# Performance work log

Hardware: AMD Instinct MI355X
Metric: run time of the kernel (lower is better)

Reference implementation:

```python
import jax, jax.numpy as jnp
import numpy as np

N_ROLES = 6
EPS = 1e-5

def _ln(x, scale, bias):
    m = jnp.mean(x, axis=-1, keepdims=True)
    v = jnp.var(x, axis=-1, keepdims=True)
    return (x - m) * jax.lax.rsqrt(v + EPS) * scale + bias

def setup_inputs() -> dict:
    key = jax.random.key(0)
    ks = jax.random.split(key, 20)
    T, B, D_OBS, H, A = 32, 1024, 256, 512, 32
    inp = {
        'rnn_states': jax.random.normal(ks[0], (B, H), jnp.float32),
        'obs': jax.random.normal(ks[1], (T, B, D_OBS), jnp.float32),
        'resets': jnp.zeros((T, B), jnp.float32),
        'available_actions': jnp.ones((T, B, A), jnp.float32),
        'role_ids': jax.random.randint(ks[2], (T, B), 0, N_ROLES, jnp.int32),
        # feature norm over obs_dim
        'fn_scale': jnp.ones((D_OBS,), jnp.float32),
        'fn_bias': jnp.zeros((D_OBS,), jnp.float32),
        # base MLP: obs_dim->512->512, each followed by LayerNorm
        'W0': jax.random.normal(ks[3], (D_OBS, H), jnp.float32) * 0.02,
        'b0': jnp.zeros((H,), jnp.float32),
        'ln0_scale': jnp.ones((H,), jnp.float32),
        'ln0_bias': jnp.zeros((H,), jnp.float32),
        'W1': jax.random.normal(ks[4], (H, H), jnp.float32) * 0.02,
        'b1': jnp.zeros((H,), jnp.float32),
        'ln1_scale': jnp.ones((H,), jnp.float32),
        'ln1_bias': jnp.zeros((H,), jnp.float32),
        # per-role routes: obs_dim->128->H (stacked over roles)
        'Wr0': jax.random.normal(ks[5], (N_ROLES, D_OBS, 128), jnp.float32) * 0.02,
        'br0': jnp.zeros((N_ROLES, 128), jnp.float32),
        'Wr1': jax.random.normal(ks[6], (N_ROLES, 128, H), jnp.float32) * 0.02,
        'br1': jnp.zeros((N_ROLES, H), jnp.float32),
        # per-role heads: H->64->32->action_dim (stacked over roles)
        'Wh0': jax.random.normal(ks[7], (N_ROLES, H, 64), jnp.float32) * 0.02,
        'bh0': jnp.zeros((N_ROLES, 64), jnp.float32),
        'Wh1': jax.random.normal(ks[8], (N_ROLES, 64, 32), jnp.float32) * 0.02,
        'bh1': jnp.zeros((N_ROLES, 32), jnp.float32),
        'Wh2': jax.random.normal(ks[9], (N_ROLES, 32, A), jnp.float32) * 0.02,
        'bh2': jnp.zeros((N_ROLES, A), jnp.float32),
    }
    return inp

def _gather_by_role(all_values, role_ids):
    # all_values: (K, T, B, F); role_ids: (T, B) -> (T, B, F)
    idx = role_ids[None, :, :, None].astype(jnp.int32)
    return jnp.take_along_axis(all_values, idx, axis=0)[0]

def reference(rnn_states, obs, resets, available_actions, role_ids,
              fn_scale, fn_bias, W0, b0, ln0_scale, ln0_bias,
              W1, b1, ln1_scale, ln1_bias,
              Wr0, br0, Wr1, br1,
              Wh0, bh0, Wh1, bh1, Wh2, bh2):
    # feature normalization on raw obs
    obs_n = _ln(obs, fn_scale, fn_bias)
    # shared base MLP (relu + LayerNorm after each Dense)
    e = _ln(jax.nn.relu(obs_n @ W0 + b0), ln0_scale, ln0_bias)
    e = _ln(jax.nn.relu(e @ W1 + b1), ln1_scale, ln1_bias)
    # per-role pre-GRU residual routes on (normalized) obs
    r = jax.nn.relu(jnp.einsum('tbi,kih->ktbh', obs_n, Wr0) + br0[:, None, None, :])
    r = jax.nn.relu(jnp.einsum('ktbh,kho->ktbo', r, Wr1) + br1[:, None, None, :])
    e = e + _gather_by_role(r, role_ids)
    # no recurrent policy configured: rnn_states pass through
    # per-role heads -> all logits (K, T, B, A)
    h = jax.nn.relu(jnp.einsum('tbh,khf->ktbf', e, Wh0) + bh0[:, None, None, :])
    h = jax.nn.relu(jnp.einsum('ktbf,kfg->ktbg', h, Wh1) + bh1[:, None, None, :])
    all_logits = jnp.einsum('ktbg,kga->ktba', h, Wh2) + bh2[:, None, None, :]
    logits = _gather_by_role(all_logits, role_ids)
    logits = jnp.where(available_actions > 0.5, logits, jnp.full_like(logits, -1e10))
    return rnn_states, logits
```

## Files before the change

### kernel.cpp

```cpp
#include <hip/hip_runtime.h>
#include <stdint.h>

typedef unsigned short u16;
typedef unsigned int u32;

using bf16x8 = __attribute__((ext_vector_type(8))) short;
using f32x4  = __attribute__((ext_vector_type(4))) float;

#define DEVINL __device__ __forceinline__

DEVINL float b2f(u16 u) { return __builtin_bit_cast(float, (u32)u << 16); }
DEVINL u16 f2b(float f) {
  u32 u = __builtin_bit_cast(u32, f);
  u += 0x7FFFu + ((u >> 16) & 1u);
  return (u16)(u >> 16);
}

DEVINL void gll16(const u16* src, u16* dst) {
  __builtin_amdgcn_global_load_lds(
      (const __attribute__((address_space(1))) void*)(uintptr_t)src,
      (__attribute__((address_space(3))) void*)(uintptr_t)dst, 16, 0, 0);
}

DEVINL void tp_tile(const float* __restrict__ s, u16* __restrict__ d,
                    int R, int C, int bx, int by, int z)
{
  __shared__ u16 tile[32][33];
  const size_t mstride = (size_t)R * C;
  s += (size_t)z * mstride;
  d += (size_t)z * mstride;
  int r0 = bx * 32, c0 = by * 32;
  int tx = threadIdx.x & 31, ty = threadIdx.x >> 5;
#pragma unroll
  for (int i = 0; i < 32; i += 8)
    tile[ty + i][tx] = f2b(s[(size_t)(r0 + ty + i) * C + (c0 + tx)]);
  __syncthreads();
#pragma unroll
  for (int i = 0; i < 32; i += 8)
    d[(size_t)(c0 + ty + i) * R + (r0 + tx)] = tile[tx][ty + i];
}

__global__ __launch_bounds__(256) void transpose_all(
    const float* W0, const float* W1, const float* Wr0, const float* Wr1, const float* Wh0,
    u16* W0t, u16* W1t, u16* Wr0t, u16* Wr1t, u16* Wh0t)
{
  int b = blockIdx.x;
  if (b < 128)      {            tp_tile(W0, W0t, 256, 512, b % 8,  b / 8, 0); }
  else if (b < 384) { b -= 128;  tp_tile(W1, W1t, 512, 512, b % 16, b / 16, 0); }
  else if (b < 576) { b -= 384;  int t = b / 8;  tp_tile(Wr0, Wr0t, 256, 128, b % 8,  t % 4,  t / 4); }
  else if (b < 960) { b -= 576;  int t = b / 4;  tp_tile(Wr1, Wr1t, 128, 512, b % 4,  t % 16, t / 16); }
  else              { b -= 960;  int t = b / 16; tp_tile(Wh0, Wh0t, 512, 64,  b % 16, t % 2,  t / 2); }
}

__global__ __launch_bounds__(256) void ln_f32_256(
    const float* __restrict__ X, const float* __restrict__ sc,
    const float* __restrict__ bi, u16* __restrict__ Y, int nrows)
{
  constexpr int D = 256, PER = 4;
  int lane = threadIdx.x & 63;
  int row = blockIdx.x * 4 + (threadIdx.x >> 6);
  if (row >= nrows) return;
  const float* xr = X + (size_t)row * D + lane * PER;
  float x[PER] __attribute__((aligned(16)));
  *(float4*)x = *(const float4*)xr;
  float s = 0.f, s2 = 0.f;
#pragma unroll
  for (int p = 0; p < PER; ++p) { s += x[p]; s2 += x[p] * x[p]; }
#pragma unroll
  for (int o = 32; o > 0; o >>= 1) { s += __shfl_xor(s, o, 64); s2 += __shfl_xor(s2, o, 64); }
  float m = s * (1.f / D);
  float v = s2 * (1.f / D) - m * m;
  float inv = rsqrtf(v + 1e-5f);
  u16 yu[PER] __attribute__((aligned(8)));
#pragma unroll
  for (int p = 0; p < PER; ++p)
    yu[p] = f2b((x[p] - m) * inv * sc[lane * PER + p] + bi[lane * PER + p]);
  *(uint2*)(Y + (size_t)row * D + lane * PER) = *(uint2*)yu;
}

#define NROLE 6
__global__ __launch_bounds__(256) void role_count(
    const int* __restrict__ rid, int* __restrict__ blkCnt)
{
  __shared__ int h[NROLE];
  if (threadIdx.x < NROLE) h[threadIdx.x] = 0;
  __syncthreads();
  int i = blockIdx.x * 256 + threadIdx.x;
  atomicAdd(&h[rid[i]], 1);
  __syncthreads();
  if (threadIdx.x < NROLE) blkCnt[blockIdx.x * NROLE + threadIdx.x] = h[threadIdx.x];
}

__global__ __launch_bounds__(256) void role_scan(
    const int* __restrict__ blkCnt, int* __restrict__ blkBase,
    int* __restrict__ baseArr, int* __restrict__ cntArr)
{
  __shared__ int c[128 * NROLE];
  __shared__ int bb[128 * NROLE];
  __shared__ int sbase[NROLE], scnt[NROLE];
  for (int i = threadIdx.x; i < 128 * NROLE; i += 256) c[i] = blkCnt[i];
  __syncthreads();
  if (threadIdx.x < NROLE) {
    int k = threadIdx.x, run = 0;
    for (int b = 0; b < 128; ++b) { bb[b * NROLE + k] = run; run += c[b * NROLE + k]; }
    scnt[k] = run;
  }
  __syncthreads();
  if (threadIdx.x == 0) {
    int r = 0;
    for (int k = 0; k < NROLE; ++k) { sbase[k] = r; r += scnt[k]; }
  }
  __syncthreads();
  if (threadIdx.x < NROLE) { baseArr[threadIdx.x] = sbase[threadIdx.x]; cntArr[threadIdx.x] = scnt[threadIdx.x]; }
  for (int i = threadIdx.x; i < 128 * NROLE; i += 256)
    blkBase[i] = bb[i] + sbase[i % NROLE];
}

__global__ __launch_bounds__(256) void role_fill(
    const int* __restrict__ rid, const int* __restrict__ blkBase, int* __restrict__ bucket)
{
  __shared__ int h[NROLE];
  if (threadIdx.x < NROLE) h[threadIdx.x] = 0;
  __syncthreads();
  int i = blockIdx.x * 256 + threadIdx.x;
  int k = rid[i];
  int pos = atomicAdd(&h[k], 1);
  bucket[blkBase[blockIdx.x * NROLE + k] + pos] = i;
}

template <int K>
__global__ __launch_bounds__(256, 2) void gemm_ln(
    const u16* __restrict__ A, const u16* __restrict__ Bt,
    const float* __restrict__ bias, const float* __restrict__ lnsc,
    const float* __restrict__ lnbi, u16* __restrict__ C)
{
  constexpr int BM = 64, BK = 64;
  __shared__ __align__(16) u16 As[BM * BK];
  __shared__ float redS[64][4];
  __shared__ float redSS[64][4];
  __shared__ float prm[1536];
  const int tid = threadIdx.x;
  const int rowBase = blockIdx.x * BM;
  const int lane = tid & 63, wave = tid >> 6;
#pragma unroll
  for (int i = tid; i < 512; i += 256) {
    prm[i] = bias[i]; prm[512 + i] = lnsc[i]; prm[1024 + i] = lnbi[i];
  }
  u32 aOff[2];
#pragma unroll
  for (int r = 0; r < 2; ++r) {
    int row = r * 32 + (tid >> 3);
    int chunk = tid & 7;
    aOff[r] = (u32)(rowBase + row) * (u32)K + (u32)((chunk ^ (row & 7)) * 8);
  }
  const int quad = lane >> 4, lm = lane & 15, l7 = lm & 7;
  const int wn = wave * 128;
  u32 bOff[8];
#pragma unroll
  for (int j = 0; j < 8; ++j)
    bOff[j] = (u32)(wn + j * 16 + lm) * (u32)K + (u32)(quad * 8);

  f32x4 acc[4][8] = {};

  for (int k0 = 0; k0 < K; k0 += BK) {
#pragma unroll
    for (int r = 0; r < 2; ++r)
      gll16(A + aOff[r] + k0, &As[r * 2048 + wave * 512]);
    __syncthreads();
#pragma unroll
    for (int kk = 0; kk < BK; kk += 32) {
      const int kc = kk >> 3;
      bf16x8 af[4], bfr[8];
#pragma unroll
      for (int i2 = 0; i2 < 4; ++i2)
        af[i2] = *(const bf16x8*)&As[(i2 * 16 + lm) * 64 + (((quad + kc) ^ l7) * 8)];
#pragma unroll
      for (int j = 0; j < 8; ++j)
        bfr[j] = *(const bf16x8*)(Bt + bOff[j] + k0 + kk);
#pragma unroll
      for (int i2 = 0; i2 < 4; ++i2)
#pragma unroll
        for (int j = 0; j < 8; ++j)
          acc[i2][j] = __builtin_amdgcn_mfma_f32_16x16x32_bf16(af[i2], bfr[j], acc[i2][j], 0, 0, 0);
    }
    __syncthreads();
  }

#pragma unroll
  for (int i2 = 0; i2 < 4; ++i2) {
#pragma unroll
    for (int r2 = 0; r2 < 4; ++r2) {
      float s = 0.f, ss = 0.f;
#pragma unroll
      for (int j = 0; j < 8; ++j) {
        float v = acc[i2][j][r2] + prm[wn + j * 16 + lm];
        v = fmaxf(v, 0.f);
        acc[i2][j][r2] = v;
        s += v; ss += v * v;
      }
#pragma unroll
      for (int o = 1; o < 16; o <<= 1) { s += __shfl_xor(s, o, 64); ss += __shfl_xor(ss, o, 64); }
      if (lm == 0) {
        int rowL = i2 * 16 + quad * 4 + r2;
        redS[rowL][wave] = s;
        redSS[rowL][wave] = ss;
      }
    }
  }
  __syncthreads();
#pragma unroll
  for (int i2 = 0; i2 < 4; ++i2) {
#pragma unroll
    for (int r2 = 0; r2 < 4; ++r2) {
      int rowL = i2 * 16 + quad * 4 + r2;
      float ts  = redS[rowL][0] + redS[rowL][1] + redS[rowL][2] + redS[rowL][3];
      float tss = redSS[rowL][0] + redSS[rowL][1] + redSS[rowL][2] + redSS[rowL][3];
      float m = ts * (1.f / 512.f);
      float var = tss * (1.f / 512.f) - m * m;
      float inv = rsqrtf(var + 1e-5f);
      size_t base = (size_t)(rowBase + rowL) * 512;
#pragma unroll
      for (int j = 0; j < 8; ++j) {
        int col = wn + j * 16 + lm;
        float y = (acc[i2][j][r2] - m) * inv * prm[512 + col] + prm[1024 + col];
        C[base + col] = f2b(y);
      }
    }
  }
}

enum { GM_GATHER = 1, GM_CONTIG = 2, GM_GATHER_ADD = 3 };

template <int BN, int MODE>
__global__ __launch_bounds__(256, 2) void gemm_bk128(
    const u16* __restrict__ A, const u16* __restrict__ Bt,
    const float* __restrict__ bias, u16* __restrict__ C,
    const u16* __restrict__ E,
    const int* __restrict__ bucket, const int* __restrict__ baseArr,
    const int* __restrict__ cntArr, int K, int ldc)
{
  constexpr int BM = 128, BK = 128;
  constexpr int NF = BN / 32;
  constexpr int AR = BM * BK / 2048;
  constexpr int BR2 = BN * BK / 2048;
  __shared__ __align__(16) u16 As[BM * BK];
  __shared__ __align__(16) u16 Bs[BN * BK];
  const int tid = threadIdx.x;

  int role = 0, rem = blockIdx.x, cnt;
  for (;;) {
    cnt = cntArr[role];
    int tiles = (cnt + BM - 1) >> 7;
    if (rem < tiles) break;
    rem -= tiles;
    if (++role >= NROLE) return;
  }
  const int limit = cnt;
  const int rowBase = rem * BM;
  const int roleBase = baseArr[role];
  const int N = gridDim.y * BN;
  const u16* BtK = Bt + (size_t)role * N * K + (size_t)blockIdx.y * BN * K;
  const float* biasK = bias + (size_t)role * N + (size_t)blockIdx.y * BN;

  const int lane = tid & 63, wave = tid >> 6;

  u32 aOff[AR];
#pragma unroll
  for (int r = 0; r < AR; ++r) {
    int row = r * 16 + (tid >> 4);
    int chunk = tid & 15;
    int i = rowBase + row;
    if (i >= limit) i = rowBase;
    int grow;
    if constexpr (MODE == GM_GATHER) grow = bucket[roleBase + i];
    else                             grow = roleBase + i;
    aOff[r] = (u32)grow * (u32)K + (u32)((chunk ^ (row & 7)) * 8);
  }
  u32 bOff[BR2];
#pragma unroll
  for (int r = 0; r < BR2; ++r) {
    int brow = r * 16 + (tid >> 4);
    int chunk = tid & 15;
    bOff[r] = (u32)brow * (u32)K + (u32)((chunk ^ (brow & 7)) * 8);
  }

  f32x4 acc[4][NF] = {};
  const int wm = (wave >> 1) * 64;
  const int wn = (wave & 1) * (NF * 16);
  const int quad = lane >> 4, lm = lane & 15, l7 = lm & 7;

  for (int k0 = 0; k0 < K; k0 += BK) {
#pragma unroll
    for (int r = 0; r < AR; ++r)
      gll16(A + aOff[r] + k0, &As[r * 2048 + wave * 512]);
#pragma unroll
    for (int r = 0; r < BR2; ++r)
      gll16(BtK + bOff[r] + k0, &Bs[r * 2048 + wave * 512]);
    __syncthreads();
#pragma unroll
    for (int kk = 0; kk < BK; kk += 32) {
      const int kc = kk >> 3;
      bf16x8 af[4], bfr[NF];
#pragma unroll
      for (int i2 = 0; i2 < 4; ++i2)
        af[i2] = *(const bf16x8*)&As[(wm + i2 * 16 + lm) * 128 + (((quad + kc) ^ l7) * 8)];
#pragma unroll
      for (int j = 0; j < NF; ++j)
        bfr[j] = *(const bf16x8*)&Bs[(wn + j * 16 + lm) * 128 + (((quad + kc) ^ l7) * 8)];
#pragma unroll
      for (int i2 = 0; i2 < 4; ++i2)
#pragma unroll
        for (int j = 0; j < NF; ++j)
          acc[i2][j] = __builtin_amdgcn_mfma_f32_16x16x32_bf16(af[i2], bfr[j], acc[i2][j], 0, 0, 0);
    }
    __syncthreads();
  }

#pragma unroll
  for (int i2 = 0; i2 < 4; ++i2) {
#pragma unroll
    for (int r2 = 0; r2 < 4; ++r2) {
      int lrow = wm + i2 * 16 + quad * 4 + r2;
      int i = rowBase + lrow;
      if (i >= limit) continue;
      size_t crow = (size_t)(roleBase + i), erow = 0;
      if constexpr (MODE == GM_GATHER_ADD) erow = (size_t)bucket[roleBase + i];
#pragma unroll
      for (int j = 0; j < NF; ++j) {
        int lcol = wn + j * 16 + lm;
        float v = fmaxf(acc[i2][j][r2] + biasK[lcol], 0.f);
        size_t col = (size_t)blockIdx.y * BN + lcol;
        if constexpr (MODE == GM_GATHER_ADD) v += b2f(E[erow * (size_t)ldc + col]);
        C[crow * (size_t)ldc + col] = f2b(v);
      }
    }
  }
}

__global__ __launch_bounds__(256) void head_tail(
    const u16* __restrict__ h0buf, const int* __restrict__ bucket,
    const int* __restrict__ baseArr,
    const float* __restrict__ Wh1, const float* __restrict__ bh1,
    const float* __restrict__ Wh2, const float* __restrict__ bh2,
    const float* __restrict__ avail, float* __restrict__ outLogits)
{
  int lane = threadIdx.x & 63;
  int p = blockIdx.x * 4 + (threadIdx.x >> 6);
  int row = bucket[p];
  int k = 0;
#pragma unroll
  for (int j = 1; j < NROLE; ++j) k += (p >= baseArr[j]);
  float h0 = b2f(h0buf[(size_t)p * 64 + lane]);
  int n = lane & 31, half = lane >> 5;
  const float* W1k = Wh1 + k * 64 * 32;
  float a1 = 0.f;
#pragma unroll
  for (int jj = 0; jj < 32; ++jj) {
    int j = half * 32 + jj;
    float hj = __shfl(h0, j, 64);
    a1 += hj * W1k[j * 32 + n];
  }
  a1 += __shfl_xor(a1, 32, 64);
  float h1 = fmaxf(a1 + bh1[k * 32 + n], 0.f);
  const float* W2k = Wh2 + k * 32 * 32;
  float a2 = 0.f;
#pragma unroll
  for (int nn = 0; nn < 32; ++nn) {
    float hn = __shfl(h1, nn, 64);
    a2 += hn * W2k[nn * 32 + n];
  }
  float logit = a2 + bh2[k * 32 + n];
  float av = avail[(size_t)row * 32 + n];
  if (av <= 0.5f) logit = -1e10f;
  if (half == 0) outLogits[(size_t)row * 32 + n] = logit;
}

extern "C" void kernel_launch(void* const* d_in, const int* in_sizes, int n_in,
                              void* d_out, int out_size, void* d_ws, size_t ws_size,
                              hipStream_t stream)
{
  const float* rnn  = (const float*)d_in[0];
  const float* obs  = (const float*)d_in[1];
  const float* avail= (const float*)d_in[3];
  const int*   rid  = (const int*)d_in[4];
  const float* fn_s = (const float*)d_in[5];
  const float* fn_b = (const float*)d_in[6];
  const float* W0   = (const float*)d_in[7];
  const float* b0   = (const float*)d_in[8];
  const float* ln0s = (const float*)d_in[9];
  const float* ln0b = (const float*)d_in[10];
  const float* W1   = (const float*)d_in[11];
  const float* b1   = (const float*)d_in[12];
  const float* ln1s = (const float*)d_in[13];
  const float* ln1b = (const float*)d_in[14];
  const float* Wr0  = (const float*)d_in[15];
  const float* br0  = (const float*)d_in[16];
  const float* Wr1  = (const float*)d_in[17];
  const float* br1  = (const float*)d_in[18];
  const float* Wh0  = (const float*)d_in[19];
  const float* bh0  = (const float*)d_in[20];
  const float* Wh1  = (const float*)d_in[21];
  const float* bh1  = (const float*)d_in[22];
  const float* Wh2  = (const float*)d_in[23];
  const float* bh2  = (const float*)d_in[24];

  const int ROWS = 32768;

  char* w = (char*)d_ws;
  auto carve = [&](size_t bytes) { char* p = w; w += (bytes + 255) & ~(size_t)255; return p; };
  u16* obs_n  = (u16*)carve((size_t)ROWS * 256 * 2);
  u16* bufA   = (u16*)carve((size_t)ROWS * 512 * 2);
  u16* bufB   = (u16*)carve((size_t)ROWS * 512 * 2);
  u16* r_buf  = (u16*)carve((size_t)ROWS * 128 * 2);
  u16* h0buf  = (u16*)carve((size_t)ROWS * 64 * 2);
  u16* W0t    = (u16*)carve((size_t)512 * 256 * 2);
  u16* W1t    = (u16*)carve((size_t)512 * 512 * 2);
  u16* Wr0t   = (u16*)carve((size_t)6 * 128 * 256 * 2);
  u16* Wr1t   = (u16*)carve((size_t)6 * 512 * 128 * 2);
  u16* Wh0t   = (u16*)carve((size_t)6 * 64 * 512 * 2);
  int* bucket = (int*)carve((size_t)ROWS * 4);
  int* blkCnt = (int*)carve((size_t)128 * NROLE * 4);
  int* blkBase= (int*)carve((size_t)128 * NROLE * 4);
  int* baseArr= (int*)carve(256);
  int* cntArr = (int*)carve(256);

  float* outLogits = (float*)d_out + (size_t)1024 * 512;

  hipMemcpyAsync(d_out, rnn, (size_t)1024 * 512 * 4, hipMemcpyDeviceToDevice, stream);

  transpose_all<<<1152, 256, 0, stream>>>(W0, W1, Wr0, Wr1, Wh0, W0t, W1t, Wr0t, Wr1t, Wh0t);

  ln_f32_256<<<8192, 256, 0, stream>>>(obs, fn_s, fn_b, obs_n, ROWS);

  role_count<<<128, 256, 0, stream>>>(rid, blkCnt);
  role_scan<<<1, 256, 0, stream>>>(blkCnt, blkBase, baseArr, cntArr);
  role_fill<<<128, 256, 0, stream>>>(rid, blkBase, bucket);

  gemm_ln<256><<<512, 256, 0, stream>>>(obs_n, W0t, b0, ln0s, ln0b, bufA);
  gemm_ln<512><<<512, 256, 0, stream>>>(bufA, W1t, b1, ln1s, ln1b, bufB);

  gemm_bk128<128, GM_GATHER><<<dim3(261, 1), 256, 0, stream>>>(
      obs_n, Wr0t, br0, r_buf, nullptr, bucket, baseArr, cntArr, 256, 128);
  gemm_bk128<128, GM_GATHER_ADD><<<dim3(261, 4), 256, 0, stream>>>(
      r_buf, Wr1t, br1, bufA, bufB, bucket, baseArr, cntArr, 128, 512);

  gemm_bk128<64, GM_CONTIG><<<dim3(261, 1), 256, 0, stream>>>(
      bufA, Wh0t, bh0, h0buf, nullptr, bucket, baseArr, cntArr, 512, 64);

  head_tail<<<8192, 256, 0, stream>>>(h0buf, bucket, baseArr, Wh1, bh1, Wh2, bh2, avail, outLogits);
}
```

Measured before the change: 310.3 us.

## Fuse per-role route and head GEMMs into one kernel; halve gemm_ln tile

Replaces the three separate per-role GEMM launches (route layer 0, route layer 1 with gather-add, head layer 0) with one fused kernel. It processes 32 role-sorted rows per block and keeps the intermediate activations in shared memory, so the r_buf and the per-role residual buffer no longer round-trip through global memory. The shared-trunk gemm_ln kernels also drop from 64- to 32-row tiles with higher occupancy bounds and twice the blocks. The trade-off is that weights are now read straight from global per block, re-read across more blocks, and small tiles lower MFMA reuse.

```diff
diff --git a/kernel.cpp b/kernel.cpp
--- a/kernel.cpp
+++ b/kernel.cpp
@@ -129,30 +129,25 @@
 }
 
 template <int K>
-__global__ __launch_bounds__(256, 2) void gemm_ln(
+__global__ __launch_bounds__(256, 4) void gemm_ln(
     const u16* __restrict__ A, const u16* __restrict__ Bt,
     const float* __restrict__ bias, const float* __restrict__ lnsc,
     const float* __restrict__ lnbi, u16* __restrict__ C)
 {
-  constexpr int BM = 64, BK = 64;
-  __shared__ __align__(16) u16 As[BM * BK];
-  __shared__ float redS[64][4];
-  __shared__ float redSS[64][4];
+  constexpr int BK = 64;
+  __shared__ __align__(16) u16 As[32 * BK];
+  __shared__ float redS[32][4];
+  __shared__ float redSS[32][4];
   __shared__ float prm[1536];
   const int tid = threadIdx.x;
-  const int rowBase = blockIdx.x * BM;
+  const int rowBase = blockIdx.x * 32;
   const int lane = tid & 63, wave = tid >> 6;
 #pragma unroll
   for (int i = tid; i < 512; i += 256) {
     prm[i] = bias[i]; prm[512 + i] = lnsc[i]; prm[1024 + i] = lnbi[i];
   }
-  u32 aOff[2];
-#pragma unroll
-  for (int r = 0; r < 2; ++r) {
-    int row = r * 32 + (tid >> 3);
-    int chunk = tid & 7;
-    aOff[r] = (u32)(rowBase + row) * (u32)K + (u32)((chunk ^ (row & 7)) * 8);
-  }
+  const int srow = tid >> 3;
+  const u32 aOff = (u32)(rowBase + srow) * (u32)K + (u32)(((tid & 7) ^ (srow & 7)) * 8);
   const int quad = lane >> 4, lm = lane & 15, l7 = lm & 7;
   const int wn = wave * 128;
   u32 bOff[8];
@@ -160,25 +155,23 @@
   for (int j = 0; j < 8; ++j)
     bOff[j] = (u32)(wn + j * 16 + lm) * (u32)K + (u32)(quad * 8);
 
-  f32x4 acc[4][8] = {};
+  f32x4 acc[2][8] = {};
 
   for (int k0 = 0; k0 < K; k0 += BK) {
-#pragma unroll
-    for (int r = 0; r < 2; ++r)
-      gll16(A + aOff[r] + k0, &As[r * 2048 + wave * 512]);
+    gll16(A + aOff + k0, &As[wave * 512]);
     __syncthreads();
 #pragma unroll
     for (int kk = 0; kk < BK; kk += 32) {
       const int kc = kk >> 3;
-      bf16x8 af[4], bfr[8];
-#pragma unroll
-      for (int i2 = 0; i2 < 4; ++i2)
+      bf16x8 af[2], bfr[8];
+#pragma unroll
+      for (int i2 = 0; i2 < 2; ++i2)
         af[i2] = *(const bf16x8*)&As[(i2 * 16 + lm) * 64 + (((quad + kc) ^ l7) * 8)];
 #pragma unroll
       for (int j = 0; j < 8; ++j)
         bfr[j] = *(const bf16x8*)(Bt + bOff[j] + k0 + kk);
 #pragma unroll
-      for (int i2 = 0; i2 < 4; ++i2)
+      for (int i2 = 0; i2 < 2; ++i2)
 #pragma unroll
         for (int j = 0; j < 8; ++j)
           acc[i2][j] = __builtin_amdgcn_mfma_f32_16x16x32_bf16(af[i2], bfr[j], acc[i2][j], 0, 0, 0);
@@ -187,14 +180,13 @@
   }
 
 #pragma unroll
-  for (int i2 = 0; i2 < 4; ++i2) {
+  for (int i2 = 0; i2 < 2; ++i2) {
 #pragma unroll
     for (int r2 = 0; r2 < 4; ++r2) {
       float s = 0.f, ss = 0.f;
 #pragma unroll
       for (int j = 0; j < 8; ++j) {
-        float v = acc[i2][j][r2] + prm[wn + j * 16 + lm];
-        v = fmaxf(v, 0.f);
+        float v = fmaxf(acc[i2][j][r2] + prm[wn + j * 16 + lm], 0.f);
         acc[i2][j][r2] = v;
         s += v; ss += v * v;
       }
@@ -209,7 +201,7 @@
   }
   __syncthreads();
 #pragma unroll
-  for (int i2 = 0; i2 < 4; ++i2) {
+  for (int i2 = 0; i2 < 2; ++i2) {
 #pragma unroll
     for (int r2 = 0; r2 < 4; ++r2) {
       int rowL = i2 * 16 + quad * 4 + r2;
@@ -229,110 +221,150 @@
   }
 }
 
-enum { GM_GATHER = 1, GM_CONTIG = 2, GM_GATHER_ADD = 3 };
-
-template <int BN, int MODE>
-__global__ __launch_bounds__(256, 2) void gemm_bk128(
-    const u16* __restrict__ A, const u16* __restrict__ Bt,
-    const float* __restrict__ bias, u16* __restrict__ C,
-    const u16* __restrict__ E,
+__global__ __launch_bounds__(256, 3) void route_head(
+    const u16* __restrict__ obs_n, const u16* __restrict__ e,
+    const u16* __restrict__ Wr0t, const float* __restrict__ br0,
+    const u16* __restrict__ Wr1t, const float* __restrict__ br1,
+    const u16* __restrict__ Wh0t, const float* __restrict__ bh0,
     const int* __restrict__ bucket, const int* __restrict__ baseArr,
-    const int* __restrict__ cntArr, int K, int ldc)
-{
-  constexpr int BM = 128, BK = 128;
-  constexpr int NF = BN / 32;
-  constexpr int AR = BM * BK / 2048;
-  constexpr int BR2 = BN * BK / 2048;
-  __shared__ __align__(16) u16 As[BM * BK];
-  __shared__ __align__(16) u16 Bs[BN * BK];
+    const int* __restrict__ cntArr, u16* __restrict__ h0buf)
+{
+  __shared__ __align__(16) u16 sm[20480];
+  __shared__ float prm[704];
   const int tid = threadIdx.x;
 
   int role = 0, rem = blockIdx.x, cnt;
   for (;;) {
     cnt = cntArr[role];
-    int tiles = (cnt + BM - 1) >> 7;
+    int tiles = (cnt + 31) >> 5;
     if (rem < tiles) break;
     rem -= tiles;
     if (++role >= NROLE) return;
   }
   const int limit = cnt;
-  const int rowBase = rem * BM;
+  const int rowBase = rem * 32;
   const int roleBase = baseArr[role];
-  const int N = gridDim.y * BN;
-  const u16* BtK = Bt + (size_t)role * N * K + (size_t)blockIdx.y * BN * K;
-  const float* biasK = bias + (size_t)role * N + (size_t)blockIdx.y * BN;
+
+  {
+    const float* s0 = br0 + role * 128;
+    const float* s1 = br1 + role * 512;
+    const float* s2 = bh0 + role * 64;
+    if (tid < 128) prm[tid] = s0[tid];
+    for (int i = tid; i < 512; i += 256) prm[128 + i] = s1[i];
+    if (tid < 64) prm[640 + tid] = s2[tid];
+  }
 
   const int lane = tid & 63, wave = tid >> 6;
-
-  u32 aOff[AR];
-#pragma unroll
-  for (int r = 0; r < AR; ++r) {
-    int row = r * 16 + (tid >> 4);
-    int chunk = tid & 15;
-    int i = rowBase + row;
+  const int quad = lane >> 4, lm = lane & 15, l7 = lm & 7;
+
+#pragma unroll
+  for (int r = 0; r < 4; ++r) {
+    int lrow = r * 8 + (tid >> 5);
+    int i = rowBase + lrow;
     if (i >= limit) i = rowBase;
-    int grow;
-    if constexpr (MODE == GM_GATHER) grow = bucket[roleBase + i];
-    else                             grow = roleBase + i;
-    aOff[r] = (u32)grow * (u32)K + (u32)((chunk ^ (row & 7)) * 8);
-  }
-  u32 bOff[BR2];
-#pragma unroll
-  for (int r = 0; r < BR2; ++r) {
-    int brow = r * 16 + (tid >> 4);
-    int chunk = tid & 15;
-    bOff[r] = (u32)brow * (u32)K + (u32)((chunk ^ (brow & 7)) * 8);
-  }
-
-  f32x4 acc[4][NF] = {};
-  const int wm = (wave >> 1) * 64;
-  const int wn = (wave & 1) * (NF * 16);
-  const int quad = lane >> 4, lm = lane & 15, l7 = lm & 7;
-
-  for (int k0 = 0; k0 < K; k0 += BK) {
-#pragma unroll
-    for (int r = 0; r < AR; ++r)
-      gll16(A + aOff[r] + k0, &As[r * 2048 + wave * 512]);
-#pragma unroll
-    for (int r = 0; r < BR2; ++r)
-      gll16(BtK + bOff[r] + k0, &Bs[r * 2048 + wave * 512]);
-    __syncthreads();
-#pragma unroll
-    for (int kk = 0; kk < BK; kk += 32) {
-      const int kc = kk >> 3;
-      bf16x8 af[4], bfr[NF];
-#pragma unroll
-      for (int i2 = 0; i2 < 4; ++i2)
-        af[i2] = *(const bf16x8*)&As[(wm + i2 * 16 + lm) * 128 + (((quad + kc) ^ l7) * 8)];
-#pragma unroll
-      for (int j = 0; j < NF; ++j)
-        bfr[j] = *(const bf16x8*)&Bs[(wn + j * 16 + lm) * 128 + (((quad + kc) ^ l7) * 8)];
-#pragma unroll
-      for (int i2 = 0; i2 < 4; ++i2)
-#pragma unroll
-        for (int j = 0; j < NF; ++j)
-          acc[i2][j] = __builtin_amdgcn_mfma_f32_16x16x32_bf16(af[i2], bfr[j], acc[i2][j], 0, 0, 0);
-    }
-    __syncthreads();
-  }
-
-#pragma unroll
-  for (int i2 = 0; i2 < 4; ++i2) {
+    int grow = bucket[roleBase + i];
+    gll16(obs_n + (u32)grow * 256u + (u32)((((tid & 31) ^ (lrow & 7)) * 8)),
+          &sm[r * 2048 + wave * 512]);
+  }
+  __syncthreads();
+
+  const int wn0 = wave * 32;
+  const u16* B0 = Wr0t + (size_t)role * 128 * 256;
+  f32x4 acc0[2][2] = {};
+#pragma unroll
+  for (int kk = 0; kk < 256; kk += 32) {
+    const int kc = kk >> 3;
+    bf16x8 af[2], bf0[2];
+#pragma unroll
+    for (int i2 = 0; i2 < 2; ++i2)
+      af[i2] = *(const bf16x8*)&sm[(i2 * 16 + lm) * 256 + (((quad + kc) ^ l7) * 8)];
+#pragma unroll
+    for (int j = 0; j < 2; ++j)
+      bf0[j] = *(const bf16x8*)(B0 + (u32)(wn0 + j * 16 + lm) * 256u + (u32)(quad * 8 + kk));
+#pragma unroll
+    for (int i2 = 0; i2 < 2; ++i2)
+#pragma unroll
+      for (int j = 0; j < 2; ++j)
+        acc0[i2][j] = __builtin_amdgcn_mfma_f32_16x16x32_bf16(af[i2], bf0[j], acc0[i2][j], 0, 0, 0);
+  }
+  u16* r1 = sm + 16384;
+#pragma unroll
+  for (int i2 = 0; i2 < 2; ++i2) {
 #pragma unroll
     for (int r2 = 0; r2 < 4; ++r2) {
-      int lrow = wm + i2 * 16 + quad * 4 + r2;
-      int i = rowBase + lrow;
+      int row = i2 * 16 + quad * 4 + r2;
+#pragma unroll
+      for (int j = 0; j < 2; ++j) {
+        int col = wn0 + j * 16 + lm;
+        float v = fmaxf(acc0[i2][j][r2] + prm[col], 0.f);
+        r1[row * 128 + (((col >> 3) ^ (row & 7)) * 8) + (col & 7)] = f2b(v);
+      }
+    }
+  }
+  __syncthreads();
+
+  const int wn1 = wave * 128;
+  const u16* B1 = Wr1t + (size_t)role * 512 * 128;
+  f32x4 acc1[2][8] = {};
+#pragma unroll
+  for (int kk = 0; kk < 128; kk += 32) {
+    const int kc = kk >> 3;
+    bf16x8 af[2], bf1[8];
+#pragma unroll
+    for (int i2 = 0; i2 < 2; ++i2)
+      af[i2] = *(const bf16x8*)&r1[(i2 * 16 + lm) * 128 + (((quad + kc) ^ l7) * 8)];
+#pragma unroll
+    for (int j = 0; j < 8; ++j)
+      bf1[j] = *(const bf16x8*)(B1 + (u32)(wn1 + j * 16 + lm) * 128u + (u32)(quad * 8 + kk));
+#pragma unroll
+    for (int i2 = 0; i2 < 2; ++i2)
+#pragma unroll
+      for (int j = 0; j < 8; ++j)
+        acc1[i2][j] = __builtin_amdgcn_mfma_f32_16x16x32_bf16(af[i2], bf1[j], acc1[i2][j], 0, 0, 0);
+  }
+#pragma unroll
+  for (int i2 = 0; i2 < 2; ++i2) {
+#pragma unroll
+    for (int r2 = 0; r2 < 4; ++r2) {
+      int row = i2 * 16 + quad * 4 + r2;
+      int i = rowBase + row;
+      int ic = (i < limit) ? i : (limit - 1);
+      u32 grow = (u32)bucket[roleBase + ic];
+#pragma unroll
+      for (int j = 0; j < 8; ++j) {
+        int col = wn1 + j * 16 + lm;
+        float v = fmaxf(acc1[i2][j][r2] + prm[128 + col], 0.f) + b2f(e[(size_t)grow * 512 + col]);
+        sm[row * 512 + (((col >> 3) ^ (row & 7)) * 8) + (col & 7)] = f2b(v);
+      }
+    }
+  }
+  __syncthreads();
+
+  const int wn2 = wave * 16;
+  const u16* B2 = Wh0t + (size_t)role * 64 * 512;
+  f32x4 acc2[2] = {};
+#pragma unroll
+  for (int kk = 0; kk < 512; kk += 32) {
+    const int kc = kk >> 3;
+    bf16x8 af[2], bf2;
+#pragma unroll
+    for (int i2 = 0; i2 < 2; ++i2)
+      af[i2] = *(const bf16x8*)&sm[(i2 * 16 + lm) * 512 + (((quad + kc) ^ l7) * 8)];
+    bf2 = *(const bf16x8*)(B2 + (u32)(wn2 + lm) * 512u + (u32)(quad * 8 + kk));
+#pragma unroll
+    for (int i2 = 0; i2 < 2; ++i2)
+      acc2[i2] = __builtin_amdgcn_mfma_f32_16x16x32_bf16(af[i2], bf2, acc2[i2], 0, 0, 0);
+  }
+#pragma unroll
+  for (int i2 = 0; i2 < 2; ++i2) {
+#pragma unroll
+    for (int r2 = 0; r2 < 4; ++r2) {
+      int row = i2 * 16 + quad * 4 + r2;
+      int i = rowBase + row;
       if (i >= limit) continue;
-      size_t crow = (size_t)(roleBase + i), erow = 0;
-      if constexpr (MODE == GM_GATHER_ADD) erow = (size_t)bucket[roleBase + i];
-#pragma unroll
-      for (int j = 0; j < NF; ++j) {
-        int lcol = wn + j * 16 + lm;
-        float v = fmaxf(acc[i2][j][r2] + biasK[lcol], 0.f);
-        size_t col = (size_t)blockIdx.y * BN + lcol;
-        if constexpr (MODE == GM_GATHER_ADD) v += b2f(E[erow * (size_t)ldc + col]);
-        C[crow * (size_t)ldc + col] = f2b(v);
-      }
+      int col = wn2 + lm;
+      float v = fmaxf(acc2[i2][r2] + prm[640 + col], 0.f);
+      h0buf[(size_t)(roleBase + i) * 64 + col] = f2b(v);
     }
   }
 }
@@ -411,7 +443,6 @@
   u16* obs_n  = (u16*)carve((size_t)ROWS * 256 * 2);
   u16* bufA   = (u16*)carve((size_t)ROWS * 512 * 2);
   u16* bufB   = (u16*)carve((size_t)ROWS * 512 * 2);
-  u16* r_buf  = (u16*)carve((size_t)ROWS * 128 * 2);
   u16* h0buf  = (u16*)carve((size_t)ROWS * 64 * 2);
   u16* W0t    = (u16*)carve((size_t)512 * 256 * 2);
   u16* W1t    = (u16*)carve((size_t)512 * 512 * 2);
@@ -436,16 +467,11 @@
   role_scan<<<1, 256, 0, stream>>>(blkCnt, blkBase, baseArr, cntArr);
   role_fill<<<128, 256, 0, stream>>>(rid, blkBase, bucket);
 
-  gemm_ln<256><<<512, 256, 0, stream>>>(obs_n, W0t, b0, ln0s, ln0b, bufA);
-  gemm_ln<512><<<512, 256, 0, stream>>>(bufA, W1t, b1, ln1s, ln1b, bufB);
-
-  gemm_bk128<128, GM_GATHER><<<dim3(261, 1), 256, 0, stream>>>(
-      obs_n, Wr0t, br0, r_buf, nullptr, bucket, baseArr, cntArr, 256, 128);
-  gemm_bk128<128, GM_GATHER_ADD><<<dim3(261, 4), 256, 0, stream>>>(
-      r_buf, Wr1t, br1, bufA, bufB, bucket, baseArr, cntArr, 128, 512);
-
-  gemm_bk128<64, GM_CONTIG><<<dim3(261, 1), 256, 0, stream>>>(
-      bufA, Wh0t, bh0, h0buf, nullptr, bucket, baseArr, cntArr, 512, 64);
+  gemm_ln<256><<<1024, 256, 0, stream>>>(obs_n, W0t, b0, ln0s, ln0b, bufA);
+  gemm_ln<512><<<1024, 256, 0, stream>>>(bufA, W1t, b1, ln1s, ln1b, bufB);
+
+  route_head<<<1029, 256, 0, stream>>>(obs_n, bufB, Wr0t, br0, Wr1t, br1, Wh0t, bh0,
+                                       bucket, baseArr, cntArr, h0buf);
 
   head_tail<<<8192, 256, 0, stream>>>(h0buf, bucket, baseArr, Wh1, bh1, Wh2, bh2, avail, outLogits);
 }
```

Result: slower. 317.6 us (+2.3%).
